# Performance work log

Measured on AMD Instinct MI355X. Metric: run time of the kernel, lower is better.

The kernel has to match this reference:

```python
import jax, jax.numpy as jnp
import numpy as np

EPS = 0.01       # perturbation radius (constructor arg)
MEAN = 0.1307    # MNIST normalize constants from the 'else' branch
SIGMA = 0.3081


def _get_bound(v, eps):
    # torch get_bound detaches eps before taking |.| and summing
    r = jnp.sum(jnp.abs(jax.lax.stop_gradient(eps)), axis=-1)
    return v + r, v - r


def _relu_zono(v, eps):
    # v: [N], eps: [N, E]. Append one fresh (zero) error column, as the torch code does.
    n = v.shape[0]
    eps = jnp.concatenate([eps, jnp.zeros((n, 1), eps.dtype)], axis=-1)  # [N, E+1]
    u, l = _get_bound(v, eps)
    denom = u - l  # = 2*sum|eps| >= 0; guard against 0 for non-crossing rows
    # slopes are created as Parameters = u/(u-l) on the first pass (detached leaf)
    slope = jax.lax.stop_gradient(u / jnp.where(denom == 0, 1.0, denom))
    # at init slope == base = u/(u-l), so the slope <= base branch is taken
    term = (1.0 - slope) * u * 0.5
    crossing = (u > 0) & (l < 0)
    dead = u <= 0
    # torch uses slope.data * values.data for the linear part, + term (term carries grad)
    v_cross = jax.lax.stop_gradient(slope * v) + term
    v_new = jnp.where(dead, 0.0, jnp.where(crossing, v_cross, v))
    eps_cross = jnp.concatenate([slope[:, None] * eps[:, :-1], term[:, None]], axis=-1)
    eps_new = jnp.where(dead[:, None], 0.0, jnp.where(crossing[:, None], eps_cross, eps))
    return v_new, eps_new


def _forward(inputs, W1, b1, W2, b2, W3, b3):
    # initial zonotope build (faithful to source: values = u + l, radii = values - l = u)
    upper = jnp.minimum(inputs + EPS, 1.0)   # upper - relu(upper - 1)
    lower = jnp.maximum(inputs - EPS, 0.0)   # relu(lower)
    values = upper + lower
    eps = jnp.diag((values - lower).flatten())  # [D, D]
    # Normalize layer (the 'else' branch)
    values = (values - MEAN) / SIGMA
    eps = eps / SIGMA
    # Flatten
    v = values.flatten()
    # Linear -> ReLU -> Linear -> ReLU -> Linear
    v = W1 @ v + b1
    eps = W1 @ eps
    v, eps = _relu_zono(v, eps)
    v = W2 @ v + b2
    eps = W2 @ eps
    v, eps = _relu_zono(v, eps)
    v = W3 @ v + b3
    eps = W3 @ eps
    u, l = _get_bound(v, eps)
    return u, l


def setup_inputs() -> dict:
    key = jax.random.key(0)
    ks = jax.random.split(key, 7)
    D, H, O = 1024, 4096, 10
    inputs = jax.random.uniform(ks[0], (1, 1, 32, 32), jnp.float32)
    W1 = jax.random.normal(ks[1], (H, D), jnp.float32) / np.float32(np.sqrt(D))
    b1 = jax.random.normal(ks[2], (H,), jnp.float32) * 0.01
    W2 = jax.random.normal(ks[3], (H, H), jnp.float32) / np.float32(np.sqrt(H))
    b2 = jax.random.normal(ks[4], (H,), jnp.float32) * 0.01
    W3 = jax.random.normal(ks[5], (O, H), jnp.float32) / np.float32(np.sqrt(H))
    b3 = jax.random.normal(ks[6], (O,), jnp.float32) * 0.01
    return {"inputs": inputs, "W1": W1, "b1": b1, "W2": W2, "b2": b2, "W3": W3, "b3": b3}


def reference(inputs, W1, b1, W2, b2, W3, b3):
    return _forward(inputs, W1, b1, W2, b2, W3, b3)
```

## Files before the change

### kernel.cpp

```cpp
#include <hip/hip_runtime.h>
#include <math.h>

#define ZEPS  0.01f
#define ZMEAN 0.1307f
#define ZSIGMA 0.3081f

constexpr int D = 1024, H = 4096, O = 10;

using short8 = __attribute__((ext_vector_type(8))) short;
using f32x4  = __attribute__((ext_vector_type(4))) float;
typedef unsigned short ushort_t;

__device__ inline unsigned short f2bf(float x) {
    unsigned int u = __float_as_uint(x);
    u += 0x7FFFu + ((u >> 16) & 1u);
    return (unsigned short)(u >> 16);
}
__device__ inline float bf2f(unsigned short h) {
    return __uint_as_float(((unsigned int)h) << 16);
}
__device__ inline unsigned int f2bf2(float a, float b) {
    return (unsigned int)f2bf(a) | ((unsigned int)f2bf(b) << 16);
}

__device__ inline void gl_lds16(const void* g, void* l) {
    __builtin_amdgcn_global_load_lds(
        (const __attribute__((address_space(1))) unsigned int*)g,
        (__attribute__((address_space(3))) unsigned int*)l, 16, 0, 0);
}

__device__ inline float zval(float xv) {
    float up = fminf(xv + ZEPS, 1.f);
    float lo = fmaxf(xv - ZEPS, 0.f);
    return (up + lo - ZMEAN) / ZSIGMA;
}
__device__ inline float zdia(float xv) {
    return fminf(xv + ZEPS, 1.f) / ZSIGMA;
}

__device__ inline void relu_params(float v, float r, float& vout, float& aout, float& tout) {
    float u = v + r, l = v - r;
    float denom = u - l;
    float slope = u / (denom == 0.f ? 1.f : denom);
    float term = (1.f - slope) * u * 0.5f;
    bool dead = (u <= 0.f);
    bool crossing = (u > 0.f) && (l < 0.f);
    vout = dead ? 0.f : (crossing ? (slope * v + term) : v);
    aout = dead ? 0.f : (crossing ? slope : 1.f);
    tout = (!dead && crossing) ? term : 0.f;
}

__global__ __launch_bounds__(256) void k_layer1(const float* __restrict__ W1, const float* __restrict__ b1,
                                                const float* __restrict__ x,
                                                float* __restrict__ v1p, float* __restrict__ a1,
                                                float* __restrict__ t1) {
    int wid = threadIdx.x >> 6, lane = threadIdx.x & 63;
    int i = blockIdx.x * 4 + wid;
    const float* row = W1 + (size_t)i * D;
    float sv = 0.f, sr = 0.f;
#pragma unroll
    for (int it = 0; it < 4; ++it) {
        int j = it * 256 + lane * 4;
        float4 w = *(const float4*)&row[j];
        float4 xx = *(const float4*)&x[j];
        sv += w.x * zval(xx.x) + w.y * zval(xx.y) + w.z * zval(xx.z) + w.w * zval(xx.w);
        sr += fabsf(w.x) * zdia(xx.x) + fabsf(w.y) * zdia(xx.y) +
              fabsf(w.z) * zdia(xx.z) + fabsf(w.w) * zdia(xx.w);
    }
#pragma unroll
    for (int m = 1; m <= 32; m <<= 1) {
        sv += __shfl_xor(sv, m, 64);
        sr += __shfl_xor(sr, m, 64);
    }
    if (lane == 0) {
        float vo, ao, to;
        relu_params(sv + b1[i], sr, vo, ao, to);
        v1p[i] = vo; a1[i] = ao; t1[i] = to;
    }
}

__global__ __launch_bounds__(256) void k_scaleT(const float* __restrict__ W1, const float* __restrict__ a1,
                                                const float* __restrict__ x,
                                                ushort_t* __restrict__ W1sT) {
    __shared__ float tile[32][33];
    int j0 = blockIdx.x * 32, k0 = blockIdx.y * 32;
    int r = threadIdx.x >> 3;
    int c = (threadIdx.x & 7) * 4;
    float4 w = *(const float4*)&W1[(size_t)(k0 + r) * D + j0 + c];
    float4 xx = *(const float4*)&x[j0 + c];
    float a = a1[k0 + r];
    tile[r][c + 0] = a * w.x * zdia(xx.x);
    tile[r][c + 1] = a * w.y * zdia(xx.y);
    tile[r][c + 2] = a * w.z * zdia(xx.z);
    tile[r][c + 3] = a * w.w * zdia(xx.w);
    __syncthreads();
    ushort4 o;
    o.x = f2bf(tile[c + 0][r]);
    o.y = f2bf(tile[c + 1][r]);
    o.z = f2bf(tile[c + 2][r]);
    o.w = f2bf(tile[c + 3][r]);
    *(ushort4*)&W1sT[(size_t)(j0 + r) * H + k0 + c] = o;
}

__global__ __launch_bounds__(256) void k_w2conv(const float* __restrict__ W2,
                                                const float* __restrict__ v1p,
                                                const float* __restrict__ t1,
                                                ushort_t* __restrict__ W2bf,
                                                float* __restrict__ v2raw,
                                                float* __restrict__ t2raw) {
    int wid = threadIdx.x >> 6, lane = threadIdx.x & 63;
    int i = blockIdx.x * 4 + wid;
    const float* row = W2 + (size_t)i * H;
    ushort_t* orow = W2bf + (size_t)i * H;
    float sv = 0.f, st = 0.f;
#pragma unroll 2
    for (int it = 0; it < 8; ++it) {
        int j = it * 512 + lane * 8;
        float4 w0 = *(const float4*)&row[j];
        float4 w1 = *(const float4*)&row[j + 4];
        float4 v0 = *(const float4*)&v1p[j];
        float4 v1 = *(const float4*)&v1p[j + 4];
        float4 t0 = *(const float4*)&t1[j];
        float4 t1v = *(const float4*)&t1[j + 4];
        sv += w0.x * v0.x + w0.y * v0.y + w0.z * v0.z + w0.w * v0.w
            + w1.x * v1.x + w1.y * v1.y + w1.z * v1.z + w1.w * v1.w;
        st += w0.x * t0.x + w0.y * t0.y + w0.z * t0.z + w0.w * t0.w
            + w1.x * t1v.x + w1.y * t1v.y + w1.z * t1v.z + w1.w * t1v.w;
        uint4 o;
        o.x = f2bf2(w0.x, w0.y);
        o.y = f2bf2(w0.z, w0.w);
        o.z = f2bf2(w1.x, w1.y);
        o.w = f2bf2(w1.z, w1.w);
        *(uint4*)&orow[j] = o;
    }
#pragma unroll
    for (int m = 1; m <= 32; m <<= 1) {
        sv += __shfl_xor(sv, m, 64);
        st += __shfl_xor(st, m, 64);
    }
    if (lane == 0) { v2raw[i] = sv; t2raw[i] = st; }
}

#define GBK 64
__global__ __launch_bounds__(512) void k_gemm_mfma(const ushort_t* __restrict__ A,
                                                   const ushort_t* __restrict__ B,
                                                   ushort_t* __restrict__ C) {
    const int N = D, K = H;
    __shared__ __align__(16) ushort_t As[3][128 * GBK];
    __shared__ __align__(16) ushort_t Bs[3][256 * GBK];
    int b = blockIdx.x;
    int ym = ((b >> 5) << 2) | (b & 3);
    int z  = (b >> 2) & 1;
    int xn = (b >> 3) & 3;
    int tid = threadIdx.x;
    int wave = tid >> 6, lane = tid & 63;
    int bm = ym * 128, bn = xn * 256;
    int kbeg = z * (K / 2);
    ushort_t* Cz = C + (size_t)z * ((size_t)H * D);
    int wm = (wave >> 2) * 64, wn = (wave & 3) * 64;

    int srow = lane >> 3, sc = lane & 7, scp = sc ^ srow;
    int r15 = lane & 15, quad = lane >> 4, key = r15 & 7;

    const int S = (K / 2) / GBK;

    const ushort_t* Abase = A + (size_t)(bm + wave * 16 + srow) * K + kbeg + scp * 8;
    const ushort_t* Bbase = B + (size_t)(bn + wave * 32 + srow) * K + kbeg + scp * 8;

    auto issue = [&](int s, int slot) {
#pragma unroll
        for (int g = 0; g < 2; ++g)
            gl_lds16(Abase + (size_t)(g * 8) * K + s * GBK,
                     &As[slot][(wave * 16 + g * 8) * GBK]);
#pragma unroll
        for (int g = 0; g < 4; ++g)
            gl_lds16(Bbase + (size_t)(g * 8) * K + s * GBK,
                     &Bs[slot][(wave * 32 + g * 8) * GBK]);
    };

    f32x4 acc[4][4];
#pragma unroll
    for (int p = 0; p < 4; ++p)
#pragma unroll
        for (int q = 0; q < 4; ++q) acc[p][q] = (f32x4){0.f, 0.f, 0.f, 0.f};

    issue(0, 0);
    issue(1, 1);
    __builtin_amdgcn_sched_barrier(0);
    asm volatile("s_waitcnt vmcnt(6)" ::: "memory");
    __builtin_amdgcn_s_barrier();
    __builtin_amdgcn_sched_barrier(0);

    for (int s = 0; s < S; ++s) {
        int slot = s % 3;
        if (s + 2 < S) issue(s + 2, (s + 2) % 3);
#pragma unroll
        for (int kk = 0; kk < 2; ++kk) {
            short8 af[4], bfr[4];
#pragma unroll
            for (int mt = 0; mt < 4; ++mt)
                af[mt] = *(const short8*)&As[slot][(wm + mt * 16 + r15) * GBK + (((kk * 4 + quad) ^ key)) * 8];
#pragma unroll
            for (int nt = 0; nt < 4; ++nt)
                bfr[nt] = *(const short8*)&Bs[slot][(wn + nt * 16 + r15) * GBK + (((kk * 4 + quad) ^ key)) * 8];
            __builtin_amdgcn_s_setprio(1);
#pragma unroll
            for (int mt = 0; mt < 4; ++mt)
#pragma unroll
                for (int nt = 0; nt < 4; ++nt)
                    acc[mt][nt] = __builtin_amdgcn_mfma_f32_16x16x32_bf16(af[mt], bfr[nt], acc[mt][nt], 0, 0, 0);
            __builtin_amdgcn_s_setprio(0);
        }
        if (s < S - 2) {
            __builtin_amdgcn_sched_barrier(0);
            asm volatile("s_waitcnt vmcnt(6)" ::: "memory");
            __builtin_amdgcn_s_barrier();
            __builtin_amdgcn_sched_barrier(0);
        } else if (s == S - 2) {
            __builtin_amdgcn_sched_barrier(0);
            asm volatile("s_waitcnt vmcnt(0)" ::: "memory");
            __builtin_amdgcn_s_barrier();
            __builtin_amdgcn_sched_barrier(0);
        }
    }

#pragma unroll
    for (int mt = 0; mt < 4; ++mt) {
        int gr = bm + wm + mt * 16 + quad * 4;
#pragma unroll
        for (int nt = 0; nt < 4; ++nt) {
            int gc = bn + wn + nt * 16 + r15;
            Cz[(size_t)(gr + 0) * N + gc] = f2bf(acc[mt][nt][0]);
            Cz[(size_t)(gr + 1) * N + gc] = f2bf(acc[mt][nt][1]);
            Cz[(size_t)(gr + 2) * N + gc] = f2bf(acc[mt][nt][2]);
            Cz[(size_t)(gr + 3) * N + gc] = f2bf(acc[mt][nt][3]);
        }
    }
}

__global__ __launch_bounds__(256) void k_relu2(const ushort_t* __restrict__ e1, const ushort_t* __restrict__ e2,
                                               const float* __restrict__ v2raw, const float* __restrict__ t2raw,
                                               const float* __restrict__ b2, const float* __restrict__ W3,
                                               float* __restrict__ v2p, float* __restrict__ a2,
                                               float* __restrict__ t2, float* __restrict__ t2col,
                                               float* __restrict__ w3s) {
    int wid = threadIdx.x >> 6, lane = threadIdx.x & 63;
    int i = blockIdx.x * 4 + wid;
    float s = 0.f;
#pragma unroll
    for (int it = 0; it < 2; ++it) {
        int j = lane * 8 + it * 512;
        ushort4 a0 = *(const ushort4*)&e1[(size_t)i * D + j];
        ushort4 a1v = *(const ushort4*)&e1[(size_t)i * D + j + 4];
        ushort4 b0 = *(const ushort4*)&e2[(size_t)i * D + j];
        ushort4 b1v = *(const ushort4*)&e2[(size_t)i * D + j + 4];
        s += fabsf(bf2f(a0.x) + bf2f(b0.x)) + fabsf(bf2f(a0.y) + bf2f(b0.y))
           + fabsf(bf2f(a0.z) + bf2f(b0.z)) + fabsf(bf2f(a0.w) + bf2f(b0.w))
           + fabsf(bf2f(a1v.x) + bf2f(b1v.x)) + fabsf(bf2f(a1v.y) + bf2f(b1v.y))
           + fabsf(bf2f(a1v.z) + bf2f(b1v.z)) + fabsf(bf2f(a1v.w) + bf2f(b1v.w));
    }
#pragma unroll
    for (int m = 1; m <= 32; m <<= 1) s += __shfl_xor(s, m, 64);
    float ve = v2raw[i];
    float te = t2raw[i];
    float vo, ao, to;
    relu_params(ve + b2[i], s + fabsf(te), vo, ao, to);
    if (lane == 0) { v2p[i] = vo; a2[i] = ao; t2[i] = to; t2col[i] = te; }
    if (lane < O) w3s[(size_t)i * O + lane] = W3[(size_t)lane * H + i] * ao;
}

__global__ __launch_bounds__(256) void k_eps3a(const ushort_t* __restrict__ e1, const ushort_t* __restrict__ e2,
                                               const float* __restrict__ w3s,
                                               float* __restrict__ pbuf) {
    int jb = blockIdx.x, ib = blockIdx.y;
    int jj = threadIdx.x & 15, s = threadIdx.x >> 4;
    int j = jb * 64 + jj * 4;
    int i0 = ib * 128 + s * 8;
    float acc[4][O];
#pragma unroll
    for (int c = 0; c < 4; ++c)
#pragma unroll
        for (int o = 0; o < O; ++o) acc[c][o] = 0.f;
    for (int ii = 0; ii < 8; ++ii) {
        int i = i0 + ii;
        ushort4 a = *(const ushort4*)&e1[(size_t)i * D + j];
        ushort4 b = *(const ushort4*)&e2[(size_t)i * D + j];
        float e0 = bf2f(a.x) + bf2f(b.x), ee1 = bf2f(a.y) + bf2f(b.y);
        float ee2 = bf2f(a.z) + bf2f(b.z), ee3 = bf2f(a.w) + bf2f(b.w);
        const float* w = &w3s[(size_t)i * O];
#pragma unroll
        for (int o = 0; o < O; ++o) {
            float wo = w[o];
            acc[0][o] += wo * e0; acc[1][o] += wo * ee1;
            acc[2][o] += wo * ee2; acc[3][o] += wo * ee3;
        }
    }
    __shared__ float sm[16][64][O];
#pragma unroll
    for (int c = 0; c < 4; ++c)
#pragma unroll
        for (int o = 0; o < O; ++o) sm[s][jj * 4 + c][o] = acc[c][o];
    __syncthreads();
    for (int idx = threadIdx.x; idx < 64 * O; idx += 256) {
        int col = idx / O, o = idx % O;
        float t = 0.f;
#pragma unroll
        for (int ss = 0; ss < 16; ++ss) t += sm[ss][col][o];
        pbuf[((size_t)o * 32 + ib) * D + jb * 64 + col] = t;
    }
}

__global__ __launch_bounds__(256) void k_final(const float* __restrict__ W3, const float* __restrict__ b3,
                                               const float* __restrict__ v2p, const float* __restrict__ a2,
                                               const float* __restrict__ t2col, const float* __restrict__ t2,
                                               const float* __restrict__ pbuf, float* __restrict__ out) {
    int o = blockIdx.x, tid = threadIdx.x;
    float s3 = 0.f;
    for (int j = tid; j < D; j += 256) {
        float t = 0.f;
#pragma unroll
        for (int ib = 0; ib < 32; ++ib) t += pbuf[((size_t)o * 32 + ib) * D + j];
        s3 += fabsf(t);
    }
    const float* row = W3 + (size_t)o * H;
    float sv = 0.f, s1 = 0.f, s2 = 0.f;
    for (int i = tid; i < H; i += 256) {
        float w = row[i];
        sv += w * v2p[i];
        s1 += w * a2[i] * t2col[i];
        s2 += w * t2[i];
    }
    __shared__ float ra[256], rb[256], rc[256], rd[256];
    ra[tid] = sv; rb[tid] = s1; rc[tid] = s2; rd[tid] = s3;
    __syncthreads();
    for (int off = 128; off; off >>= 1) {
        if (tid < off) {
            ra[tid] += ra[tid + off]; rb[tid] += rb[tid + off];
            rc[tid] += rc[tid + off]; rd[tid] += rd[tid + off];
        }
        __syncthreads();
    }
    if (tid == 0) {
        float v3 = ra[0] + b3[o];
        float rr = rd[0] + fabsf(rb[0]) + fabsf(rc[0]);
        out[o] = v3 + rr;
        out[O + o] = v3 - rr;
    }
}

extern "C" void kernel_launch(void* const* d_in, const int* in_sizes, int n_in,
                              void* d_out, int out_size, void* d_ws, size_t ws_size,
                              hipStream_t stream) {
    const float* x  = (const float*)d_in[0];
    const float* W1 = (const float*)d_in[1];
    const float* b1 = (const float*)d_in[2];
    const float* W2 = (const float*)d_in[3];
    const float* b2 = (const float*)d_in[4];
    const float* W3 = (const float*)d_in[5];
    const float* b3 = (const float*)d_in[6];
    float* out = (float*)d_out;

    float* p = (float*)d_ws;
    float* v1p    = p; p += H;
    float* a1     = p; p += H;
    float* t1     = p; p += H;
    float* t2col  = p; p += H;
    float* v2p    = p; p += H;
    float* a2     = p; p += H;
    float* t2     = p; p += H;
    float* v2raw  = p; p += H;
    float* t2raw  = p; p += H;
    float* w3s    = p; p += H * O + 8;
    float* pbuf   = p; p += 32 * O * D;
    ushort_t* eps2  = (ushort_t*)p;
    ushort_t* W1sT  = eps2 + (size_t)2 * H * D;
    ushort_t* W2bf  = W1sT + (size_t)H * D;
    ushort_t* eps2b = eps2 + (size_t)H * D;

    k_layer1<<<H / 4, 256, 0, stream>>>(W1, b1, x, v1p, a1, t1);
    k_scaleT<<<dim3(D / 32, H / 32), 256, 0, stream>>>(W1, a1, x, W1sT);
    k_w2conv<<<H / 4, 256, 0, stream>>>(W2, v1p, t1, W2bf, v2raw, t2raw);
    k_gemm_mfma<<<256, 512, 0, stream>>>(W2bf, W1sT, eps2);
    k_relu2<<<H / 4, 256, 0, stream>>>(eps2, eps2b, v2raw, t2raw, b2, W3, v2p, a2, t2, t2col, w3s);
    k_eps3a<<<dim3(D / 64, 32), 256, 0, stream>>>(eps2, eps2b, w3s, pbuf);
    k_final<<<O, 256, 0, stream>>>(W3, b3, v2p, a2, t2col, t2, pbuf, out);
}
```

Baseline: 217.1 us.

## Fuse prep kernels, enlarge GEMM tiles to 256x256, atomically reduce eps3 partials

Merges the W1 scale-transpose, the W2 bf16 conversion and a zeroing pass for the eps3 reduction buffer into one launch, saving a kernel launch. The MFMA GEMM moves from 128x256 tiles with a 3-stage pipeline to 256x256 tiles with double buffering. Each tile is computed in four quadrant phases, with A and B staging interleaved across them, which raises data reuse but halves the block count to 128. The eps3 partial sums are now accumulated with atomicAdd instead of a 32-way partial buffer that k_final reduced, which adds atomic contention and makes the summation order nondeterministic.

Result: slower. 261.2 us (+20.3%).

```diff
diff --git a/kernel.cpp b/kernel.cpp
--- a/kernel.cpp
+++ b/kernel.cpp
@@ -79,66 +79,67 @@
     }
 }
 
-__global__ __launch_bounds__(256) void k_scaleT(const float* __restrict__ W1, const float* __restrict__ a1,
-                                                const float* __restrict__ x,
-                                                ushort_t* __restrict__ W1sT) {
-    __shared__ float tile[32][33];
-    int j0 = blockIdx.x * 32, k0 = blockIdx.y * 32;
-    int r = threadIdx.x >> 3;
-    int c = (threadIdx.x & 7) * 4;
-    float4 w = *(const float4*)&W1[(size_t)(k0 + r) * D + j0 + c];
-    float4 xx = *(const float4*)&x[j0 + c];
-    float a = a1[k0 + r];
-    tile[r][c + 0] = a * w.x * zdia(xx.x);
-    tile[r][c + 1] = a * w.y * zdia(xx.y);
-    tile[r][c + 2] = a * w.z * zdia(xx.z);
-    tile[r][c + 3] = a * w.w * zdia(xx.w);
-    __syncthreads();
-    ushort4 o;
-    o.x = f2bf(tile[c + 0][r]);
-    o.y = f2bf(tile[c + 1][r]);
-    o.z = f2bf(tile[c + 2][r]);
-    o.w = f2bf(tile[c + 3][r]);
-    *(ushort4*)&W1sT[(size_t)(j0 + r) * H + k0 + c] = o;
-}
-
-__global__ __launch_bounds__(256) void k_w2conv(const float* __restrict__ W2,
-                                                const float* __restrict__ v1p,
-                                                const float* __restrict__ t1,
-                                                ushort_t* __restrict__ W2bf,
-                                                float* __restrict__ v2raw,
-                                                float* __restrict__ t2raw) {
-    int wid = threadIdx.x >> 6, lane = threadIdx.x & 63;
-    int i = blockIdx.x * 4 + wid;
-    const float* row = W2 + (size_t)i * H;
-    ushort_t* orow = W2bf + (size_t)i * H;
-    float sv = 0.f, st = 0.f;
+__global__ __launch_bounds__(256) void k_fused2(const float* __restrict__ W1, const float* __restrict__ a1,
+                                                const float* __restrict__ x, ushort_t* __restrict__ W1sT,
+                                                const float* __restrict__ W2, const float* __restrict__ v1p,
+                                                const float* __restrict__ t1, ushort_t* __restrict__ W2bf,
+                                                float* __restrict__ v2raw, float* __restrict__ t2raw,
+                                                float* __restrict__ pbufR) {
+    int b = blockIdx.x;
+    if (b < 4096) {
+        __shared__ float tile[32][33];
+        int j0 = (b & 31) * 32, k0 = (b >> 5) * 32;
+        int r = threadIdx.x >> 3;
+        int c = (threadIdx.x & 7) * 4;
+        float4 w = *(const float4*)&W1[(size_t)(k0 + r) * D + j0 + c];
+        float4 xx = *(const float4*)&x[j0 + c];
+        float a = a1[k0 + r];
+        tile[r][c + 0] = a * w.x * zdia(xx.x);
+        tile[r][c + 1] = a * w.y * zdia(xx.y);
+        tile[r][c + 2] = a * w.z * zdia(xx.z);
+        tile[r][c + 3] = a * w.w * zdia(xx.w);
+        __syncthreads();
+        ushort4 o;
+        o.x = f2bf(tile[c + 0][r]);
+        o.y = f2bf(tile[c + 1][r]);
+        o.z = f2bf(tile[c + 2][r]);
+        o.w = f2bf(tile[c + 3][r]);
+        *(ushort4*)&W1sT[(size_t)(j0 + r) * H + k0 + c] = o;
+    } else if (b < 5120) {
+        int wid = threadIdx.x >> 6, lane = threadIdx.x & 63;
+        int i = (b - 4096) * 4 + wid;
+        const float* row = W2 + (size_t)i * H;
+        ushort_t* orow = W2bf + (size_t)i * H;
+        float sv = 0.f, st = 0.f;
 #pragma unroll 2
-    for (int it = 0; it < 8; ++it) {
-        int j = it * 512 + lane * 8;
-        float4 w0 = *(const float4*)&row[j];
-        float4 w1 = *(const float4*)&row[j + 4];
-        float4 v0 = *(const float4*)&v1p[j];
-        float4 v1 = *(const float4*)&v1p[j + 4];
-        float4 t0 = *(const float4*)&t1[j];
-        float4 t1v = *(const float4*)&t1[j + 4];
-        sv += w0.x * v0.x + w0.y * v0.y + w0.z * v0.z + w0.w * v0.w
-            + w1.x * v1.x + w1.y * v1.y + w1.z * v1.z + w1.w * v1.w;
-        st += w0.x * t0.x + w0.y * t0.y + w0.z * t0.z + w0.w * t0.w
-            + w1.x * t1v.x + w1.y * t1v.y + w1.z * t1v.z + w1.w * t1v.w;
-        uint4 o;
-        o.x = f2bf2(w0.x, w0.y);
-        o.y = f2bf2(w0.z, w0.w);
-        o.z = f2bf2(w1.x, w1.y);
-        o.w = f2bf2(w1.z, w1.w);
-        *(uint4*)&orow[j] = o;
-    }
-#pragma unroll
-    for (int m = 1; m <= 32; m <<= 1) {
-        sv += __shfl_xor(sv, m, 64);
-        st += __shfl_xor(st, m, 64);
-    }
-    if (lane == 0) { v2raw[i] = sv; t2raw[i] = st; }
+        for (int it = 0; it < 8; ++it) {
+            int j = it * 512 + lane * 8;
+            float4 w0 = *(const float4*)&row[j];
+            float4 w1 = *(const float4*)&row[j + 4];
+            float4 v0 = *(const float4*)&v1p[j];
+            float4 v1 = *(const float4*)&v1p[j + 4];
+            float4 t0 = *(const float4*)&t1[j];
+            float4 t1v = *(const float4*)&t1[j + 4];
+            sv += w0.x * v0.x + w0.y * v0.y + w0.z * v0.z + w0.w * v0.w
+                + w1.x * v1.x + w1.y * v1.y + w1.z * v1.z + w1.w * v1.w;
+            st += w0.x * t0.x + w0.y * t0.y + w0.z * t0.z + w0.w * t0.w
+                + w1.x * t1v.x + w1.y * t1v.y + w1.z * t1v.z + w1.w * t1v.w;
+            uint4 o;
+            o.x = f2bf2(w0.x, w0.y);
+            o.y = f2bf2(w0.z, w0.w);
+            o.z = f2bf2(w1.x, w1.y);
+            o.w = f2bf2(w1.z, w1.w);
+            *(uint4*)&orow[j] = o;
+        }
+#pragma unroll
+        for (int m = 1; m <= 32; m <<= 1) {
+            sv += __shfl_xor(sv, m, 64);
+            st += __shfl_xor(st, m, 64);
+        }
+        if (lane == 0) { v2raw[i] = sv; t2raw[i] = st; }
+    } else {
+        for (int k = threadIdx.x; k < O * D; k += 256) pbufR[k] = 0.f;
+    }
 }
 
 #define GBK 64
@@ -146,96 +147,166 @@
                                                    const ushort_t* __restrict__ B,
                                                    ushort_t* __restrict__ C) {
     const int N = D, K = H;
-    __shared__ __align__(16) ushort_t As[3][128 * GBK];
-    __shared__ __align__(16) ushort_t Bs[3][256 * GBK];
-    int b = blockIdx.x;
-    int ym = ((b >> 5) << 2) | (b & 3);
-    int z  = (b >> 2) & 1;
-    int xn = (b >> 3) & 3;
+    __shared__ __align__(16) ushort_t As[2][256 * GBK];
+    __shared__ __align__(16) ushort_t Bs[2][256 * GBK];
+    int orig = blockIdx.x;
+    int b = (orig & 7) * 16 + (orig >> 3);
+    int ym = b >> 3;
+    int xn = (b >> 1) & 3;
+    int z  = b & 1;
     int tid = threadIdx.x;
     int wave = tid >> 6, lane = tid & 63;
-    int bm = ym * 128, bn = xn * 256;
+    int bm = ym * 256, bn = xn * 256;
     int kbeg = z * (K / 2);
     ushort_t* Cz = C + (size_t)z * ((size_t)H * D);
-    int wm = (wave >> 2) * 64, wn = (wave & 3) * 64;
-
-    int srow = lane >> 3, sc = lane & 7, scp = sc ^ srow;
+    int wm = (wave >> 2) * 128, wn = (wave & 3) * 64;
+
+    int srow = lane >> 3, scp = (lane & 7) ^ srow;
     int r15 = lane & 15, quad = lane >> 4, key = r15 & 7;
 
     const int S = (K / 2) / GBK;
 
-    const ushort_t* Abase = A + (size_t)(bm + wave * 16 + srow) * K + kbeg + scp * 8;
-    const ushort_t* Bbase = B + (size_t)(bn + wave * 32 + srow) * K + kbeg + scp * 8;
-
-    auto issue = [&](int s, int slot) {
-#pragma unroll
-        for (int g = 0; g < 2; ++g)
-            gl_lds16(Abase + (size_t)(g * 8) * K + s * GBK,
-                     &As[slot][(wave * 16 + g * 8) * GBK]);
+    const ushort_t* Ab = A + (size_t)(bm + wave * 32 + srow) * K + kbeg + scp * 8;
+    const ushort_t* Bb = B + (size_t)(bn + wave * 32 + srow) * K + kbeg + scp * 8;
+
+    auto stageA = [&](int t, int buf) {
 #pragma unroll
         for (int g = 0; g < 4; ++g)
-            gl_lds16(Bbase + (size_t)(g * 8) * K + s * GBK,
-                     &Bs[slot][(wave * 32 + g * 8) * GBK]);
+            gl_lds16(Ab + (size_t)(g * 8) * K + t * GBK, &As[buf][(wave * 32 + g * 8) * GBK]);
     };
-
-    f32x4 acc[4][4];
-#pragma unroll
-    for (int p = 0; p < 4; ++p)
+    auto stageB = [&](int t, int buf) {
+#pragma unroll
+        for (int g = 0; g < 4; ++g)
+            gl_lds16(Bb + (size_t)(g * 8) * K + t * GBK, &Bs[buf][(wave * 32 + g * 8) * GBK]);
+    };
+
+    f32x4 acc[8][4];
+#pragma unroll
+    for (int p = 0; p < 8; ++p)
 #pragma unroll
         for (int q = 0; q < 4; ++q) acc[p][q] = (f32x4){0.f, 0.f, 0.f, 0.f};
 
-    issue(0, 0);
-    issue(1, 1);
+    stageA(0, 0);
+    stageB(0, 0);
     __builtin_amdgcn_sched_barrier(0);
-    asm volatile("s_waitcnt vmcnt(6)" ::: "memory");
+    asm volatile("s_waitcnt vmcnt(0)" ::: "memory");
     __builtin_amdgcn_s_barrier();
     __builtin_amdgcn_sched_barrier(0);
 
-    for (int s = 0; s < S; ++s) {
-        int slot = s % 3;
-        if (s + 2 < S) issue(s + 2, (s + 2) % 3);
-#pragma unroll
-        for (int kk = 0; kk < 2; ++kk) {
-            short8 af[4], bfr[4];
+    for (int t = 0; t < S; ++t) {
+        int buf = t & 1, nbuf = buf ^ 1;
+        short8 af[4][2], bf[2][2];
+
+        if (t + 1 < S) stageA(t + 1, nbuf);
+#pragma unroll
+        for (int mt = 0; mt < 4; ++mt)
+#pragma unroll
+            for (int kk = 0; kk < 2; ++kk)
+                af[mt][kk] = *(const short8*)&As[buf][(wm + mt * 16 + r15) * GBK + (((kk * 4 + quad) ^ key)) * 8];
+#pragma unroll
+        for (int nt = 0; nt < 2; ++nt)
+#pragma unroll
+            for (int kk = 0; kk < 2; ++kk)
+                bf[nt][kk] = *(const short8*)&Bs[buf][(wn + nt * 16 + r15) * GBK + (((kk * 4 + quad) ^ key)) * 8];
+        __builtin_amdgcn_s_barrier();
+        asm volatile("s_waitcnt lgkmcnt(0)" ::: "memory");
+        __builtin_amdgcn_sched_barrier(0);
+        __builtin_amdgcn_s_setprio(1);
+#pragma unroll
+        for (int kk = 0; kk < 2; ++kk)
 #pragma unroll
             for (int mt = 0; mt < 4; ++mt)
-                af[mt] = *(const short8*)&As[slot][(wm + mt * 16 + r15) * GBK + (((kk * 4 + quad) ^ key)) * 8];
-#pragma unroll
-            for (int nt = 0; nt < 4; ++nt)
-                bfr[nt] = *(const short8*)&Bs[slot][(wn + nt * 16 + r15) * GBK + (((kk * 4 + quad) ^ key)) * 8];
-            __builtin_amdgcn_s_setprio(1);
+#pragma unroll
+                for (int nt = 0; nt < 2; ++nt)
+                    acc[mt][nt] = __builtin_amdgcn_mfma_f32_16x16x32_bf16(af[mt][kk], bf[nt][kk], acc[mt][nt], 0, 0, 0);
+        __builtin_amdgcn_s_setprio(0);
+        __builtin_amdgcn_s_barrier();
+
+        if (t + 1 < S) stageB(t + 1, nbuf);
+#pragma unroll
+        for (int nt = 0; nt < 2; ++nt)
+#pragma unroll
+            for (int kk = 0; kk < 2; ++kk)
+                bf[nt][kk] = *(const short8*)&Bs[buf][(wn + 32 + nt * 16 + r15) * GBK + (((kk * 4 + quad) ^ key)) * 8];
+        __builtin_amdgcn_s_barrier();
+        asm volatile("s_waitcnt lgkmcnt(0)" ::: "memory");
+        __builtin_amdgcn_sched_barrier(0);
+        __builtin_amdgcn_s_setprio(1);
+#pragma unroll
+        for (int kk = 0; kk < 2; ++kk)
 #pragma unroll
             for (int mt = 0; mt < 4; ++mt)
 #pragma unroll
-                for (int nt = 0; nt < 4; ++nt)
-                    acc[mt][nt] = __builtin_amdgcn_mfma_f32_16x16x32_bf16(af[mt], bfr[nt], acc[mt][nt], 0, 0, 0);
-            __builtin_amdgcn_s_setprio(0);
+                for (int nt = 0; nt < 2; ++nt)
+                    acc[mt][2 + nt] = __builtin_amdgcn_mfma_f32_16x16x32_bf16(af[mt][kk], bf[nt][kk], acc[mt][2 + nt], 0, 0, 0);
+        __builtin_amdgcn_s_setprio(0);
+        __builtin_amdgcn_s_barrier();
+
+#pragma unroll
+        for (int mt = 0; mt < 4; ++mt)
+#pragma unroll
+            for (int kk = 0; kk < 2; ++kk)
+                af[mt][kk] = *(const short8*)&As[buf][(wm + 64 + mt * 16 + r15) * GBK + (((kk * 4 + quad) ^ key)) * 8];
+#pragma unroll
+        for (int nt = 0; nt < 2; ++nt)
+#pragma unroll
+            for (int kk = 0; kk < 2; ++kk)
+                bf[nt][kk] = *(const short8*)&Bs[buf][(wn + nt * 16 + r15) * GBK + (((kk * 4 + quad) ^ key)) * 8];
+        __builtin_amdgcn_s_barrier();
+        asm volatile("s_waitcnt lgkmcnt(0)" ::: "memory");
+        __builtin_amdgcn_sched_barrier(0);
+        __builtin_amdgcn_s_setprio(1);
+#pragma unroll
+        for (int kk = 0; kk < 2; ++kk)
+#pragma unroll
+            for (int mt = 0; mt < 4; ++mt)
+#pragma unroll
+                for (int nt = 0; nt < 2; ++nt)
+                    acc[4 + mt][nt] = __builtin_amdgcn_mfma_f32_16x16x32_bf16(af[mt][kk], bf[nt][kk], acc[4 + mt][nt], 0, 0, 0);
+        __builtin_amdgcn_s_setprio(0);
+        __builtin_amdgcn_s_barrier();
+
+#pragma unroll
+        for (int nt = 0; nt < 2; ++nt)
+#pragma unroll
+            for (int kk = 0; kk < 2; ++kk)
+                bf[nt][kk] = *(const short8*)&Bs[buf][(wn + 32 + nt * 16 + r15) * GBK + (((kk * 4 + quad) ^ key)) * 8];
+        __builtin_amdgcn_s_barrier();
+        asm volatile("s_waitcnt lgkmcnt(0)" ::: "memory");
+        __builtin_amdgcn_sched_barrier(0);
+        __builtin_amdgcn_s_setprio(1);
+#pragma unroll
+        for (int kk = 0; kk < 2; ++kk)
+#pragma unroll
+            for (int mt = 0; mt < 4; ++mt)
+#pragma unroll
+                for (int nt = 0; nt < 2; ++nt)
+                    acc[4 + mt][2 + nt] = __builtin_amdgcn_mfma_f32_16x16x32_bf16(af[mt][kk], bf[nt][kk], acc[4 + mt][2 + nt], 0, 0, 0);
+        __builtin_amdgcn_s_setprio(0);
+
+        __builtin_amdgcn_sched_barrier(0);
+        asm volatile("s_waitcnt vmcnt(0)" ::: "memory");
+        __builtin_amdgcn_s_barrier();
+        __builtin_amdgcn_sched_barrier(0);
+    }
+
+#pragma unroll
+    for (int mh = 0; mh < 2; ++mh)
+#pragma unroll
+        for (int mt = 0; mt < 4; ++mt) {
+            int gr = bm + wm + mh * 64 + mt * 16 + quad * 4;
+#pragma unroll
+            for (int nh = 0; nh < 2; ++nh)
+#pragma unroll
+                for (int nt = 0; nt < 2; ++nt) {
+                    int gc = bn + wn + nh * 32 + nt * 16 + r15;
+                    f32x4 a = acc[mh * 4 + mt][nh * 2 + nt];
+                    Cz[(size_t)(gr + 0) * N + gc] = f2bf(a[0]);
+                    Cz[(size_t)(gr + 1) * N + gc] = f2bf(a[1]);
+                    Cz[(size_t)(gr + 2) * N + gc] = f2bf(a[2]);
+                    Cz[(size_t)(gr + 3) * N + gc] = f2bf(a[3]);
+                }
         }
-        if (s < S - 2) {
-            __builtin_amdgcn_sched_barrier(0);
-            asm volatile("s_waitcnt vmcnt(6)" ::: "memory");
-            __builtin_amdgcn_s_barrier();
-            __builtin_amdgcn_sched_barrier(0);
-        } else if (s == S - 2) {
-            __builtin_amdgcn_sched_barrier(0);
-            asm volatile("s_waitcnt vmcnt(0)" ::: "memory");
-            __builtin_amdgcn_s_barrier();
-            __builtin_amdgcn_sched_barrier(0);
-        }
-    }
-
-#pragma unroll
-    for (int mt = 0; mt < 4; ++mt) {
-        int gr = bm + wm + mt * 16 + quad * 4;
-#pragma unroll
-        for (int nt = 0; nt < 4; ++nt) {
-            int gc = bn + wn + nt * 16 + r15;
-            Cz[(size_t)(gr + 0) * N + gc] = f2bf(acc[mt][nt][0]);
-            Cz[(size_t)(gr + 1) * N + gc] = f2bf(acc[mt][nt][1]);
-            Cz[(size_t)(gr + 2) * N + gc] = f2bf(acc[mt][nt][2]);
-            Cz[(size_t)(gr + 3) * N + gc] = f2bf(acc[mt][nt][3]);
-        }
-    }
 }
 
 __global__ __launch_bounds__(256) void k_relu2(const ushort_t* __restrict__ e1, const ushort_t* __restrict__ e2,
@@ -271,7 +342,7 @@
 
 __global__ __launch_bounds__(256) void k_eps3a(const ushort_t* __restrict__ e1, const ushort_t* __restrict__ e2,
                                                const float* __restrict__ w3s,
-                                               float* __restrict__ pbuf) {
+                                               float* __restrict__ pbufR) {
     int jb = blockIdx.x, ib = blockIdx.y;
     int jj = threadIdx.x & 15, s = threadIdx.x >> 4;
     int j = jb * 64 + jj * 4;
@@ -306,22 +377,17 @@
         float t = 0.f;
 #pragma unroll
         for (int ss = 0; ss < 16; ++ss) t += sm[ss][col][o];
-        pbuf[((size_t)o * 32 + ib) * D + jb * 64 + col] = t;
+        atomicAdd(&pbufR[(size_t)o * D + jb * 64 + col], t);
     }
 }
 
 __global__ __launch_bounds__(256) void k_final(const float* __restrict__ W3, const float* __restrict__ b3,
                                                const float* __restrict__ v2p, const float* __restrict__ a2,
                                                const float* __restrict__ t2col, const float* __restrict__ t2,
-                                               const float* __restrict__ pbuf, float* __restrict__ out) {
+                                               const float* __restrict__ pbufR, float* __restrict__ out) {
     int o = blockIdx.x, tid = threadIdx.x;
     float s3 = 0.f;
-    for (int j = tid; j < D; j += 256) {
-        float t = 0.f;
-#pragma unroll
-        for (int ib = 0; ib < 32; ++ib) t += pbuf[((size_t)o * 32 + ib) * D + j];
-        s3 += fabsf(t);
-    }
+    for (int j = tid; j < D; j += 256) s3 += fabsf(pbufR[(size_t)o * D + j]);
     const float* row = W3 + (size_t)o * H;
     float sv = 0.f, s1 = 0.f, s2 = 0.f;
     for (int i = tid; i < H; i += 256) {
@@ -371,17 +437,16 @@
     float* v2raw  = p; p += H;
     float* t2raw  = p; p += H;
     float* w3s    = p; p += H * O + 8;
-    float* pbuf   = p; p += 32 * O * D;
+    float* pbufR  = p; p += O * D + 8;
     ushort_t* eps2  = (ushort_t*)p;
     ushort_t* W1sT  = eps2 + (size_t)2 * H * D;
     ushort_t* W2bf  = W1sT + (size_t)H * D;
     ushort_t* eps2b = eps2 + (size_t)H * D;
 
     k_layer1<<<H / 4, 256, 0, stream>>>(W1, b1, x, v1p, a1, t1);
-    k_scaleT<<<dim3(D / 32, H / 32), 256, 0, stream>>>(W1, a1, x, W1sT);
-    k_w2conv<<<H / 4, 256, 0, stream>>>(W2, v1p, t1, W2bf, v2raw, t2raw);
-    k_gemm_mfma<<<256, 512, 0, stream>>>(W2bf, W1sT, eps2);
+    k_fused2<<<5121, 256, 0, stream>>>(W1, a1, x, W1sT, W2, v1p, t1, W2bf, v2raw, t2raw, pbufR);
+    k_gemm_mfma<<<128, 512, 0, stream>>>(W2bf, W1sT, eps2);
     k_relu2<<<H / 4, 256, 0, stream>>>(eps2, eps2b, v2raw, t2raw, b2, W3, v2p, a2, t2, t2col, w3s);
-    k_eps3a<<<dim3(D / 64, 32), 256, 0, stream>>>(eps2, eps2b, w3s, pbuf);
-    k_final<<<O, 256, 0, stream>>>(W3, b3, v2p, a2, t2col, t2, pbuf, out);
-}
+    k_eps3a<<<dim3(D / 64, 32), 256, 0, stream>>>(eps2, eps2b, w3s, pbufR);
+    k_final<<<O, 256, 0, stream>>>(W3, b3, v2p, a2, t2col, t2, pbufR, out);
+}
```

## Merge prep kernels, retile GEMM to 128x128 double-buffer, atomic partial sums

Applied to the files above, without the earlier changes.

The W2 bf16 conversion moves into a combined pre-kernel alongside layer-1 and a zeroing of the partial buffer. The W2 matvec and the W1 scale-transpose are merged into one mid kernel. The MFMA GEMM changes from 512-thread 128x256 tiles with a triple-buffered, hand-tuned waitcnt pipeline to 256-thread 128x128 tiles with a simple double buffer, __syncthreads and a remapped block order. The eps3 partial sums now use atomicAdd into one buffer instead of 32 slices. This cuts kernel launches and the final reduction, but the simpler GEMM pipeline and the W2 matvec now reading fp32 W2 a second time may cost time.

New measurement: 223.5 us. 3.0% more time.

```diff
diff --git a/kernel.cpp b/kernel.cpp
--- a/kernel.cpp
+++ b/kernel.cpp
@@ -50,132 +50,145 @@
     tout = (!dead && crossing) ? term : 0.f;
 }
 
-__global__ __launch_bounds__(256) void k_layer1(const float* __restrict__ W1, const float* __restrict__ b1,
-                                                const float* __restrict__ x,
-                                                float* __restrict__ v1p, float* __restrict__ a1,
-                                                float* __restrict__ t1) {
-    int wid = threadIdx.x >> 6, lane = threadIdx.x & 63;
-    int i = blockIdx.x * 4 + wid;
-    const float* row = W1 + (size_t)i * D;
-    float sv = 0.f, sr = 0.f;
-#pragma unroll
-    for (int it = 0; it < 4; ++it) {
-        int j = it * 256 + lane * 4;
-        float4 w = *(const float4*)&row[j];
-        float4 xx = *(const float4*)&x[j];
-        sv += w.x * zval(xx.x) + w.y * zval(xx.y) + w.z * zval(xx.z) + w.w * zval(xx.w);
-        sr += fabsf(w.x) * zdia(xx.x) + fabsf(w.y) * zdia(xx.y) +
-              fabsf(w.z) * zdia(xx.z) + fabsf(w.w) * zdia(xx.w);
-    }
-#pragma unroll
-    for (int m = 1; m <= 32; m <<= 1) {
-        sv += __shfl_xor(sv, m, 64);
-        sr += __shfl_xor(sr, m, 64);
-    }
-    if (lane == 0) {
-        float vo, ao, to;
-        relu_params(sv + b1[i], sr, vo, ao, to);
-        v1p[i] = vo; a1[i] = ao; t1[i] = to;
-    }
-}
-
-__global__ __launch_bounds__(256) void k_scaleT(const float* __restrict__ W1, const float* __restrict__ a1,
-                                                const float* __restrict__ x,
-                                                ushort_t* __restrict__ W1sT) {
-    __shared__ float tile[32][33];
-    int j0 = blockIdx.x * 32, k0 = blockIdx.y * 32;
-    int r = threadIdx.x >> 3;
-    int c = (threadIdx.x & 7) * 4;
-    float4 w = *(const float4*)&W1[(size_t)(k0 + r) * D + j0 + c];
-    float4 xx = *(const float4*)&x[j0 + c];
-    float a = a1[k0 + r];
-    tile[r][c + 0] = a * w.x * zdia(xx.x);
-    tile[r][c + 1] = a * w.y * zdia(xx.y);
-    tile[r][c + 2] = a * w.z * zdia(xx.z);
-    tile[r][c + 3] = a * w.w * zdia(xx.w);
-    __syncthreads();
-    ushort4 o;
-    o.x = f2bf(tile[c + 0][r]);
-    o.y = f2bf(tile[c + 1][r]);
-    o.z = f2bf(tile[c + 2][r]);
-    o.w = f2bf(tile[c + 3][r]);
-    *(ushort4*)&W1sT[(size_t)(j0 + r) * H + k0 + c] = o;
-}
-
-__global__ __launch_bounds__(256) void k_w2conv(const float* __restrict__ W2,
-                                                const float* __restrict__ v1p,
-                                                const float* __restrict__ t1,
-                                                ushort_t* __restrict__ W2bf,
-                                                float* __restrict__ v2raw,
-                                                float* __restrict__ t2raw) {
-    int wid = threadIdx.x >> 6, lane = threadIdx.x & 63;
-    int i = blockIdx.x * 4 + wid;
-    const float* row = W2 + (size_t)i * H;
-    ushort_t* orow = W2bf + (size_t)i * H;
-    float sv = 0.f, st = 0.f;
+__global__ __launch_bounds__(256) void k_pre(const float* __restrict__ W1, const float* __restrict__ b1,
+                                             const float* __restrict__ x,
+                                             float* __restrict__ v1p, float* __restrict__ a1,
+                                             float* __restrict__ t1,
+                                             const float* __restrict__ W2, ushort_t* __restrict__ W2bf,
+                                             float* __restrict__ pbufR) {
+    int b = blockIdx.x;
+    if (b < 2048) {
+        const float* src = W2 + (size_t)b * 8192;
+        ushort_t* dst = W2bf + (size_t)b * 8192;
+#pragma unroll
+        for (int it = 0; it < 4; ++it) {
+            int j = it * 2048 + threadIdx.x * 8;
+            float4 w0 = *(const float4*)&src[j];
+            float4 w1 = *(const float4*)&src[j + 4];
+            uint4 o;
+            o.x = f2bf2(w0.x, w0.y);
+            o.y = f2bf2(w0.z, w0.w);
+            o.z = f2bf2(w1.x, w1.y);
+            o.w = f2bf2(w1.z, w1.w);
+            *(uint4*)&dst[j] = o;
+        }
+    } else if (b < 3072) {
+        int wid = threadIdx.x >> 6, lane = threadIdx.x & 63;
+        int i = (b - 2048) * 4 + wid;
+        const float* row = W1 + (size_t)i * D;
+        float sv = 0.f, sr = 0.f;
+#pragma unroll
+        for (int it = 0; it < 4; ++it) {
+            int j = it * 256 + lane * 4;
+            float4 w = *(const float4*)&row[j];
+            float4 xx = *(const float4*)&x[j];
+            sv += w.x * zval(xx.x) + w.y * zval(xx.y) + w.z * zval(xx.z) + w.w * zval(xx.w);
+            sr += fabsf(w.x) * zdia(xx.x) + fabsf(w.y) * zdia(xx.y) +
+                  fabsf(w.z) * zdia(xx.z) + fabsf(w.w) * zdia(xx.w);
+        }
+#pragma unroll
+        for (int m = 1; m <= 32; m <<= 1) {
+            sv += __shfl_xor(sv, m, 64);
+            sr += __shfl_xor(sr, m, 64);
+        }
+        if (lane == 0) {
+            float vo, ao, to;
+            relu_params(sv + b1[i], sr, vo, ao, to);
+            v1p[i] = vo; a1[i] = ao; t1[i] = to;
+        }
+    } else {
+        for (int k = threadIdx.x; k < O * D; k += 256) pbufR[k] = 0.f;
+    }
+}
+
+__global__ __launch_bounds__(256) void k_mid(const float* __restrict__ W1, const float* __restrict__ a1,
+                                             const float* __restrict__ x, ushort_t* __restrict__ W1sT,
+                                             const float* __restrict__ W2, const float* __restrict__ v1p,
+                                             const float* __restrict__ t1,
+                                             float* __restrict__ v2raw, float* __restrict__ t2raw) {
+    int b = blockIdx.x;
+    if (b < 1024) {
+        int wid = threadIdx.x >> 6, lane = threadIdx.x & 63;
+        int i = b * 4 + wid;
+        const float* row = W2 + (size_t)i * H;
+        float sv = 0.f, st = 0.f;
 #pragma unroll 2
-    for (int it = 0; it < 8; ++it) {
-        int j = it * 512 + lane * 8;
-        float4 w0 = *(const float4*)&row[j];
-        float4 w1 = *(const float4*)&row[j + 4];
-        float4 v0 = *(const float4*)&v1p[j];
-        float4 v1 = *(const float4*)&v1p[j + 4];
-        float4 t0 = *(const float4*)&t1[j];
-        float4 t1v = *(const float4*)&t1[j + 4];
-        sv += w0.x * v0.x + w0.y * v0.y + w0.z * v0.z + w0.w * v0.w
-            + w1.x * v1.x + w1.y * v1.y + w1.z * v1.z + w1.w * v1.w;
-        st += w0.x * t0.x + w0.y * t0.y + w0.z * t0.z + w0.w * t0.w
-            + w1.x * t1v.x + w1.y * t1v.y + w1.z * t1v.z + w1.w * t1v.w;
-        uint4 o;
-        o.x = f2bf2(w0.x, w0.y);
-        o.y = f2bf2(w0.z, w0.w);
-        o.z = f2bf2(w1.x, w1.y);
-        o.w = f2bf2(w1.z, w1.w);
-        *(uint4*)&orow[j] = o;
-    }
-#pragma unroll
-    for (int m = 1; m <= 32; m <<= 1) {
-        sv += __shfl_xor(sv, m, 64);
-        st += __shfl_xor(st, m, 64);
-    }
-    if (lane == 0) { v2raw[i] = sv; t2raw[i] = st; }
+        for (int it = 0; it < 8; ++it) {
+            int j = it * 512 + lane * 8;
+            float4 w0 = *(const float4*)&row[j];
+            float4 w1 = *(const float4*)&row[j + 4];
+            float4 v0 = *(const float4*)&v1p[j];
+            float4 v1 = *(const float4*)&v1p[j + 4];
+            float4 t0 = *(const float4*)&t1[j];
+            float4 t1v = *(const float4*)&t1[j + 4];
+            sv += w0.x * v0.x + w0.y * v0.y + w0.z * v0.z + w0.w * v0.w
+                + w1.x * v1.x + w1.y * v1.y + w1.z * v1.z + w1.w * v1.w;
+            st += w0.x * t0.x + w0.y * t0.y + w0.z * t0.z + w0.w * t0.w
+                + w1.x * t1v.x + w1.y * t1v.y + w1.z * t1v.z + w1.w * t1v.w;
+        }
+#pragma unroll
+        for (int m = 1; m <= 32; m <<= 1) {
+            sv += __shfl_xor(sv, m, 64);
+            st += __shfl_xor(st, m, 64);
+        }
+        if (lane == 0) { v2raw[i] = sv; t2raw[i] = st; }
+    } else {
+        __shared__ float tile[32][33];
+        int bb = b - 1024;
+        int j0 = (bb & 31) * 32, k0 = (bb >> 5) * 32;
+        int r = threadIdx.x >> 3;
+        int c = (threadIdx.x & 7) * 4;
+        float4 w = *(const float4*)&W1[(size_t)(k0 + r) * D + j0 + c];
+        float4 xx = *(const float4*)&x[j0 + c];
+        float a = a1[k0 + r];
+        tile[r][c + 0] = a * w.x * zdia(xx.x);
+        tile[r][c + 1] = a * w.y * zdia(xx.y);
+        tile[r][c + 2] = a * w.z * zdia(xx.z);
+        tile[r][c + 3] = a * w.w * zdia(xx.w);
+        __syncthreads();
+        ushort4 o;
+        o.x = f2bf(tile[c + 0][r]);
+        o.y = f2bf(tile[c + 1][r]);
+        o.z = f2bf(tile[c + 2][r]);
+        o.w = f2bf(tile[c + 3][r]);
+        *(ushort4*)&W1sT[(size_t)(j0 + r) * H + k0 + c] = o;
+    }
 }
 
 #define GBK 64
-__global__ __launch_bounds__(512) void k_gemm_mfma(const ushort_t* __restrict__ A,
+__global__ __launch_bounds__(256) void k_gemm_mfma(const ushort_t* __restrict__ A,
                                                    const ushort_t* __restrict__ B,
                                                    ushort_t* __restrict__ C) {
     const int N = D, K = H;
-    __shared__ __align__(16) ushort_t As[3][128 * GBK];
-    __shared__ __align__(16) ushort_t Bs[3][256 * GBK];
-    int b = blockIdx.x;
-    int ym = ((b >> 5) << 2) | (b & 3);
-    int z  = (b >> 2) & 1;
-    int xn = (b >> 3) & 3;
+    __shared__ __align__(16) ushort_t As[2][128 * GBK];
+    __shared__ __align__(16) ushort_t Bs[2][128 * GBK];
+    int orig = blockIdx.x;
+    int b = (orig & 7) * 64 + (orig >> 3);
+    int z  = b >> 8;
+    int xn = (b >> 5) & 7;
+    int ym = b & 31;
     int tid = threadIdx.x;
     int wave = tid >> 6, lane = tid & 63;
-    int bm = ym * 128, bn = xn * 256;
+    int bm = ym * 128, bn = xn * 128;
     int kbeg = z * (K / 2);
     ushort_t* Cz = C + (size_t)z * ((size_t)H * D);
-    int wm = (wave >> 2) * 64, wn = (wave & 3) * 64;
-
-    int srow = lane >> 3, sc = lane & 7, scp = sc ^ srow;
+    int wm = (wave >> 1) * 64, wn = (wave & 1) * 64;
+
+    int srow = lane >> 3, scp = (lane & 7) ^ srow;
     int r15 = lane & 15, quad = lane >> 4, key = r15 & 7;
 
     const int S = (K / 2) / GBK;
 
-    const ushort_t* Abase = A + (size_t)(bm + wave * 16 + srow) * K + kbeg + scp * 8;
-    const ushort_t* Bbase = B + (size_t)(bn + wave * 32 + srow) * K + kbeg + scp * 8;
-
-    auto issue = [&](int s, int slot) {
-#pragma unroll
-        for (int g = 0; g < 2; ++g)
-            gl_lds16(Abase + (size_t)(g * 8) * K + s * GBK,
-                     &As[slot][(wave * 16 + g * 8) * GBK]);
+    const ushort_t* Ab = A + (size_t)(bm + wave * 32 + srow) * K + kbeg + scp * 8;
+    const ushort_t* Bb = B + (size_t)(bn + wave * 32 + srow) * K + kbeg + scp * 8;
+
+    auto issue = [&](int t, int buf) {
 #pragma unroll
         for (int g = 0; g < 4; ++g)
-            gl_lds16(Bbase + (size_t)(g * 8) * K + s * GBK,
-                     &Bs[slot][(wave * 32 + g * 8) * GBK]);
+            gl_lds16(Ab + (size_t)(g * 8) * K + t * GBK, &As[buf][(wave * 32 + g * 8) * GBK]);
+#pragma unroll
+        for (int g = 0; g < 4; ++g)
+            gl_lds16(Bb + (size_t)(g * 8) * K + t * GBK, &Bs[buf][(wave * 32 + g * 8) * GBK]);
     };
 
     f32x4 acc[4][4];
@@ -185,43 +198,27 @@
         for (int q = 0; q < 4; ++q) acc[p][q] = (f32x4){0.f, 0.f, 0.f, 0.f};
 
     issue(0, 0);
-    issue(1, 1);
-    __builtin_amdgcn_sched_barrier(0);
-    asm volatile("s_waitcnt vmcnt(6)" ::: "memory");
-    __builtin_amdgcn_s_barrier();
-    __builtin_amdgcn_sched_barrier(0);
-
-    for (int s = 0; s < S; ++s) {
-        int slot = s % 3;
-        if (s + 2 < S) issue(s + 2, (s + 2) % 3);
+    __syncthreads();
+
+    for (int t = 0; t < S; ++t) {
+        int buf = t & 1, nbuf = buf ^ 1;
+        if (t + 1 < S) issue(t + 1, nbuf);
 #pragma unroll
         for (int kk = 0; kk < 2; ++kk) {
             short8 af[4], bfr[4];
 #pragma unroll
             for (int mt = 0; mt < 4; ++mt)
-                af[mt] = *(const short8*)&As[slot][(wm + mt * 16 + r15) * GBK + (((kk * 4 + quad) ^ key)) * 8];
+                af[mt] = *(const short8*)&As[buf][(wm + mt * 16 + r15) * GBK + (((kk * 4 + quad) ^ key)) * 8];
 #pragma unroll
             for (int nt = 0; nt < 4; ++nt)
-                bfr[nt] = *(const short8*)&Bs[slot][(wn + nt * 16 + r15) * GBK + (((kk * 4 + quad) ^ key)) * 8];
-            __builtin_amdgcn_s_setprio(1);
+                bfr[nt] = *(const short8*)&Bs[buf][(wn + nt * 16 + r15) * GBK + (((kk * 4 + quad) ^ key)) * 8];
 #pragma unroll
             for (int mt = 0; mt < 4; ++mt)
 #pragma unroll
                 for (int nt = 0; nt < 4; ++nt)
                     acc[mt][nt] = __builtin_amdgcn_mfma_f32_16x16x32_bf16(af[mt], bfr[nt], acc[mt][nt], 0, 0, 0);
-            __builtin_amdgcn_s_setprio(0);
-        }
-        if (s < S - 2) {
-            __builtin_amdgcn_sched_barrier(0);
-            asm volatile("s_waitcnt vmcnt(6)" ::: "memory");
-            __builtin_amdgcn_s_barrier();
-            __builtin_amdgcn_sched_barrier(0);
-        } else if (s == S - 2) {
-            __builtin_amdgcn_sched_barrier(0);
-            asm volatile("s_waitcnt vmcnt(0)" ::: "memory");
-            __builtin_amdgcn_s_barrier();
-            __builtin_amdgcn_sched_barrier(0);
-        }
+        }
+        __syncthreads();
     }
 
 #pragma unroll
@@ -271,7 +268,7 @@
 
 __global__ __launch_bounds__(256) void k_eps3a(const ushort_t* __restrict__ e1, const ushort_t* __restrict__ e2,
                                                const float* __restrict__ w3s,
-                                               float* __restrict__ pbuf) {
+                                               float* __restrict__ pbufR) {
     int jb = blockIdx.x, ib = blockIdx.y;
     int jj = threadIdx.x & 15, s = threadIdx.x >> 4;
     int j = jb * 64 + jj * 4;
@@ -306,22 +303,17 @@
         float t = 0.f;
 #pragma unroll
         for (int ss = 0; ss < 16; ++ss) t += sm[ss][col][o];
-        pbuf[((size_t)o * 32 + ib) * D + jb * 64 + col] = t;
+        atomicAdd(&pbufR[(size_t)o * D + jb * 64 + col], t);
     }
 }
 
 __global__ __launch_bounds__(256) void k_final(const float* __restrict__ W3, const float* __restrict__ b3,
                                                const float* __restrict__ v2p, const float* __restrict__ a2,
                                                const float* __restrict__ t2col, const float* __restrict__ t2,
-                                               const float* __restrict__ pbuf, float* __restrict__ out) {
+                                               const float* __restrict__ pbufR, float* __restrict__ out) {
     int o = blockIdx.x, tid = threadIdx.x;
     float s3 = 0.f;
-    for (int j = tid; j < D; j += 256) {
-        float t = 0.f;
-#pragma unroll
-        for (int ib = 0; ib < 32; ++ib) t += pbuf[((size_t)o * 32 + ib) * D + j];
-        s3 += fabsf(t);
-    }
+    for (int j = tid; j < D; j += 256) s3 += fabsf(pbufR[(size_t)o * D + j]);
     const float* row = W3 + (size_t)o * H;
     float sv = 0.f, s1 = 0.f, s2 = 0.f;
     for (int i = tid; i < H; i += 256) {
@@ -371,17 +363,16 @@
     float* v2raw  = p; p += H;
     float* t2raw  = p; p += H;
     float* w3s    = p; p += H * O + 8;
-    float* pbuf   = p; p += 32 * O * D;
+    float* pbufR  = p; p += O * D + 8;
     ushort_t* eps2  = (ushort_t*)p;
     ushort_t* W1sT  = eps2 + (size_t)2 * H * D;
     ushort_t* W2bf  = W1sT + (size_t)H * D;
     ushort_t* eps2b = eps2 + (size_t)H * D;
 
-    k_layer1<<<H / 4, 256, 0, stream>>>(W1, b1, x, v1p, a1, t1);
-    k_scaleT<<<dim3(D / 32, H / 32), 256, 0, stream>>>(W1, a1, x, W1sT);
-    k_w2conv<<<H / 4, 256, 0, stream>>>(W2, v1p, t1, W2bf, v2raw, t2raw);
-    k_gemm_mfma<<<256, 512, 0, stream>>>(W2bf, W1sT, eps2);
+    k_pre<<<3073, 256, 0, stream>>>(W1, b1, x, v1p, a1, t1, W2, W2bf, pbufR);
+    k_mid<<<5120, 256, 0, stream>>>(W1, a1, x, W1sT, W2, v1p, t1, v2raw, t2raw);
+    k_gemm_mfma<<<512, 256, 0, stream>>>(W2bf, W1sT, eps2);
     k_relu2<<<H / 4, 256, 0, stream>>>(eps2, eps2b, v2raw, t2raw, b2, W3, v2p, a2, t2, t2col, w3s);
-    k_eps3a<<<dim3(D / 64, 32), 256, 0, stream>>>(eps2, eps2b, w3s, pbuf);
-    k_final<<<O, 256, 0, stream>>>(W3, b3, v2p, a2, t2col, t2, pbuf, out);
-}
+    k_eps3a<<<dim3(D / 64, 32), 256, 0, stream>>>(eps2, eps2b, w3s, pbufR);
+    k_final<<<O, 256, 0, stream>>>(W3, b3, v2p, a2, t2col, t2, pbufR, out);
+}
```
